# Performance work log

Measured on AMD Instinct MI355X. Metric: run time of the kernel, lower is better.

The kernel has to match this reference:

```python
import jax, jax.numpy as jnp
import numpy as np

DIM = 1024
D_SRC = 1024
H = 16
HD = DIM // H
SCALE = 1.0 / np.sqrt(DIM)  # module uses 1/sqrt(internal_dim), not head_dim


def setup_inputs() -> dict:
    key = jax.random.key(0)
    ks = jax.random.split(key, 7)
    B, T = 2, 2048
    Q = jax.random.normal(ks[0], (B, T, DIM), dtype=jnp.float32)
    K = jax.random.normal(ks[1], (B, T, D_SRC), dtype=jnp.float32)
    V = jax.random.normal(ks[2], (B, T, D_SRC), dtype=jnp.float32)
    # torch nn.Linear weights: (out_features, in_features); y = x @ W.T
    s = 0.02
    Wq = jax.random.normal(ks[3], (DIM, DIM), dtype=jnp.float32) * s
    Wk = jax.random.normal(ks[4], (DIM, D_SRC), dtype=jnp.float32) * s
    Wv = jax.random.normal(ks[5], (DIM, D_SRC), dtype=jnp.float32) * s
    Wo = jax.random.normal(ks[6], (DIM, DIM), dtype=jnp.float32) * s
    return {"Q": Q, "K": K, "V": V, "Wq": Wq, "Wk": Wk, "Wv": Wv, "Wo": Wo}


def _split_heads(x):  # (B,T,DIM) -> (B,H,T,HD)
    B, T, _ = x.shape
    return x.reshape(B, T, H, HD).transpose(0, 2, 1, 3)


def reference(Q, K, V, Wq, Wk, Wv, Wo):
    B, T, _ = Q.shape
    q = _split_heads(Q @ Wq.T)
    k = _split_heads(K @ Wk.T)
    v = _split_heads(V @ Wv.T)
    att = jnp.einsum('bhid,bhjd->bhij', q, k) * SCALE
    causal = jnp.tril(jnp.ones((T, T), dtype=bool))
    att = jnp.where(causal[None, None], att, -jnp.inf)
    att = jax.nn.softmax(att, axis=-1)
    y = jnp.einsum('bhij,bhjd->bhid', att, v)
    y = y.transpose(0, 2, 1, 3).reshape(B, T, DIM)
    y = y @ Wo.T
    return y, att
```

## Files before the change

kernel.cpp:

```cpp
#include <hip/hip_runtime.h>
#include <hip/hip_bf16.h>

#define Bb 2
#define Tt 2048
#define DIMd 1024
#define Hh 16
#define HDh 64
#define MTOK (Bb * Tt)
#define NSCALE 0.03125f

typedef __attribute__((ext_vector_type(8))) short bf16x8;
typedef __attribute__((ext_vector_type(4))) float floatx4;

__device__ __forceinline__ unsigned short f2bf(float f) {
    union { float f; unsigned int u; } a; a.f = f;
    const unsigned int u = a.u;
    return (unsigned short)((u + 0x7FFFu + ((u >> 16) & 1u)) >> 16);
}

__device__ __forceinline__ void gl_lds16(const void* g, void* l) {
    __builtin_amdgcn_global_load_lds((const __attribute__((address_space(1))) void*)g,
                                     (__attribute__((address_space(3))) void*)l, 16, 0, 0);
}

__global__ __launch_bounds__(256) void cvt_all(
    const float* __restrict__ s0, const float* __restrict__ s1, const float* __restrict__ s2,
    const float* __restrict__ s3, const float* __restrict__ s4, const float* __restrict__ s5,
    const float* __restrict__ s6,
    unsigned short* __restrict__ d0, unsigned short* __restrict__ d1, unsigned short* __restrict__ d2,
    unsigned short* __restrict__ d3, unsigned short* __restrict__ d4, unsigned short* __restrict__ d5,
    unsigned short* __restrict__ d6) {
    const int blk = blockIdx.x;
    const float* src; unsigned short* dst; int rb;
    if (blk < 12288) {
        const int r = blk >> 12;
        rb  = blk & 4095;
        src = (r == 0) ? s0 : ((r == 1) ? s1 : s2);
        dst = (r == 0) ? d0 : ((r == 1) ? d1 : d2);
    } else {
        const int r = (blk - 12288) >> 10;
        rb  = blk & 1023;
        src = (r == 0) ? s3 : ((r == 1) ? s4 : ((r == 2) ? s5 : s6));
        dst = (r == 0) ? d3 : ((r == 1) ? d4 : ((r == 2) ? d5 : d6));
    }
    const int i = (rb * 256 + threadIdx.x) * 4;
    const float4 v = *(const float4*)(src + i);
    ushort4 o;
    o.x = f2bf(v.x); o.y = f2bf(v.y); o.z = f2bf(v.z); o.w = f2bf(v.w);
    *(ushort4*)(dst + i) = o;
}

template <int BF16OUT>
__device__ __forceinline__ void gemm_tile(unsigned short* As, unsigned short* Bs,
                                          const unsigned short* __restrict__ A,
                                          const unsigned short* __restrict__ W,
                                          void* __restrict__ Cv,
                                          int N, int K, int m0, int n0) {
    const int tid  = threadIdx.x;
    const int wave = tid >> 6;
    const int lane = tid & 63;
    const int wm = (wave >> 1) * 64;
    const int wn = (wave & 1) * 64;
    const int qd = lane >> 4;
    const int ln16 = lane & 15;
    const int x7 = ln16 & 7;

    floatx4 acc[4][4];
#pragma unroll
    for (int mi = 0; mi < 4; ++mi)
#pragma unroll
        for (int ni = 0; ni < 4; ++ni) acc[mi][ni] = (floatx4){0.f, 0.f, 0.f, 0.f};

    for (int k0 = 0; k0 < K; k0 += 64) {
#pragma unroll
        for (int t = 0; t < 4; ++t) {
            const int c   = t * 256 + wave * 64 + lane;
            const int row = c >> 3;
            const int col = ((c & 7) ^ (row & 7)) * 8;
            gl_lds16(A + (size_t)(m0 + row) * K + k0 + col, &As[c * 8]);
            gl_lds16(W + (size_t)(n0 + row) * K + k0 + col, &Bs[c * 8]);
        }
        __syncthreads();

#pragma unroll
        for (int ks = 0; ks < 2; ++ks) {
            bf16x8 af[4], bfr[4];
#pragma unroll
            for (int mi = 0; mi < 4; ++mi)
                af[mi] = *(const bf16x8*)&As[(wm + mi * 16 + ln16) * 64 + (((ks * 4 + qd) ^ x7) * 8)];
#pragma unroll
            for (int ni = 0; ni < 4; ++ni)
                bfr[ni] = *(const bf16x8*)&Bs[(wn + ni * 16 + ln16) * 64 + (((ks * 4 + qd) ^ x7) * 8)];
            __builtin_amdgcn_s_setprio(1);
#pragma unroll
            for (int mi = 0; mi < 4; ++mi)
#pragma unroll
                for (int ni = 0; ni < 4; ++ni)
                    acc[mi][ni] = __builtin_amdgcn_mfma_f32_16x16x32_bf16(af[mi], bfr[ni], acc[mi][ni], 0, 0, 0);
            __builtin_amdgcn_s_setprio(0);
        }
        __syncthreads();
    }

#pragma unroll
    for (int mi = 0; mi < 4; ++mi)
#pragma unroll
        for (int ni = 0; ni < 4; ++ni) {
            const int gn = n0 + wn + ni * 16 + ln16;
#pragma unroll
            for (int r = 0; r < 4; ++r) {
                const int gm = m0 + wm + mi * 16 + qd * 4 + r;
                if (BF16OUT)
                    ((unsigned short*)Cv)[(size_t)gm * N + gn] = f2bf(acc[mi][ni][r]);
                else
                    ((float*)Cv)[(size_t)gm * N + gn] = acc[mi][ni][r];
            }
        }
}

__global__ __launch_bounds__(256) void gemm_proj3(
    const unsigned short* __restrict__ Qb, const unsigned short* __restrict__ Wqb, unsigned short* __restrict__ qp,
    const unsigned short* __restrict__ Kb, const unsigned short* __restrict__ Wkb, unsigned short* __restrict__ kp,
    const unsigned short* __restrict__ Vb, const unsigned short* __restrict__ Wvb, unsigned short* __restrict__ vt) {
    __shared__ unsigned short As[128 * 64];
    __shared__ unsigned short Bs[128 * 64];
    const int bid = blockIdx.x;
    if (bid < 256) {
        gemm_tile<1>(As, Bs, Qb, Wqb, qp, DIMd, DIMd, (bid >> 3) * 128, (bid & 7) * 128);
    } else if (bid < 512) {
        const int r = bid - 256;
        gemm_tile<1>(As, Bs, Kb, Wkb, kp, DIMd, DIMd, (r >> 3) * 128, (r & 7) * 128);
    } else {
        const int r = bid - 512;
        gemm_tile<1>(As, Bs, Wvb, Vb, vt, MTOK, DIMd, (r >> 5) * 128, (r & 31) * 128);
    }
}

__global__ __launch_bounds__(256) void gemm_o_rescale(const unsigned short* __restrict__ ymid,
                                                      const unsigned short* __restrict__ Wob,
                                                      float* __restrict__ y,
                                                      float* __restrict__ att,
                                                      const float* __restrict__ lws) {
    __shared__ unsigned short As[128 * 64];
    __shared__ unsigned short Bs[128 * 64];
    const int bid = blockIdx.x;
    if (bid < 256) {
        gemm_tile<0>(As, Bs, ymid, Wob, y, DIMd, DIMd, (bid >> 3) * 128, (bid & 7) * 128);
        return;
    }
    const int rb  = bid - 256;
    const int tid = threadIdx.x;
#pragma unroll
    for (int rr = 0; rr < 16; ++rr) {
        const int row = rb * 16 + rr;
        const int i   = row & (Tt - 1);
        const float inv = 1.f / lws[row];
        float4* arow = (float4*)(att + (size_t)row * Tt);
#pragma unroll
        for (int q = 0; q < 2; ++q) {
            const int f4 = tid + q * 256;
            const int j  = f4 * 4;
            float4 v;
            if (j <= i) {
                v = arow[f4];
                v.x = (j + 0 <= i) ? v.x * inv : 0.f;
                v.y = (j + 1 <= i) ? v.y * inv : 0.f;
                v.z = (j + 2 <= i) ? v.z * inv : 0.f;
                v.w = (j + 3 <= i) ? v.w * inv : 0.f;
            } else {
                v = make_float4(0.f, 0.f, 0.f, 0.f);
            }
            arow[f4] = v;
        }
    }
}

#define PSTR 72

__global__ __launch_bounds__(256) void fused_attn(const unsigned short* __restrict__ qp,
                                                  const unsigned short* __restrict__ kp,
                                                  const unsigned short* __restrict__ vt,
                                                  float* __restrict__ att,
                                                  unsigned short* __restrict__ ymid,
                                                  float* __restrict__ lws) {
    __shared__ unsigned short Ks[64 * 64];
    __shared__ unsigned short Vs[64 * 64];
    __shared__ unsigned short Ps[64 * PSTR];

    const int bid = blockIdx.x;
    const int bh  = bid & 31;
    const int it  = 31 - (bid >> 5);
    const int h   = bh & (Hh - 1);
    const int b   = bh >> 4;
    const int tid  = threadIdx.x;
    const int w    = tid >> 6;
    const int lane = tid & 63;
    const int qd   = lane >> 4;
    const int ln16 = lane & 15;
    const int i0   = it * 64;
    const int ig   = i0 + w * 16 + ln16;

    bf16x8 qf[2];
    {
        const unsigned short* qrow = qp + (size_t)(b * Tt + ig) * DIMd + h * HDh;
        qf[0] = *(const bf16x8*)(qrow + qd * 8);
        qf[1] = *(const bf16x8*)(qrow + 32 + qd * 8);
    }

    floatx4 oacc[4];
#pragma unroll
    for (int dt = 0; dt < 4; ++dt) oacc[dt] = (floatx4){0.f, 0.f, 0.f, 0.f};
    float lsum = 0.f;

    unsigned short* Pw = &Ps[w * 16 * PSTR];
    float* arow = att + ((size_t)bh * Tt + ig) * Tt;

    for (int jt = 0; jt <= it; ++jt) {
        const int j0 = jt * 64;
        __syncthreads();

#pragma unroll
        for (int t = 0; t < 2; ++t) {
            const int c   = w * 128 + t * 64 + lane;
            const int row = c >> 3;
            const int cb  = c & 7;
            const int col8 = ((cb ^ (row & 7)) * 8);
            gl_lds16(kp + (size_t)(b * Tt + j0 + row) * DIMd + h * HDh + col8, &Ks[c * 8]);
            gl_lds16(vt + (size_t)(h * HDh + row) * MTOK + b * Tt + j0 + col8, &Vs[c * 8]);
        }
        __syncthreads();

        floatx4 sacc[4];
#pragma unroll
        for (int ct = 0; ct < 4; ++ct) sacc[ct] = (floatx4){0.f, 0.f, 0.f, 0.f};
        __builtin_amdgcn_s_setprio(1);
#pragma unroll
        for (int ks = 0; ks < 2; ++ks)
#pragma unroll
            for (int ct = 0; ct < 4; ++ct) {
                const int row = ct * 16 + ln16;
                const bf16x8 kf = *(const bf16x8*)&Ks[row * 64 + (((ks * 4 + qd) ^ (row & 7)) * 8)];
                sacc[ct] = __builtin_amdgcn_mfma_f32_16x16x32_bf16(kf, qf[ks], sacc[ct], 0, 0, 0);
            }
        __builtin_amdgcn_s_setprio(0);

        float rs = 0.f;
#pragma unroll
        for (int ct = 0; ct < 4; ++ct) {
            const int jb = j0 + ct * 16 + qd * 4;
            float4 ev;
            {
                const float e0 = (jb + 0 <= ig) ? __expf(sacc[ct][0] * NSCALE) : 0.f;
                const float e1 = (jb + 1 <= ig) ? __expf(sacc[ct][1] * NSCALE) : 0.f;
                const float e2 = (jb + 2 <= ig) ? __expf(sacc[ct][2] * NSCALE) : 0.f;
                const float e3 = (jb + 3 <= ig) ? __expf(sacc[ct][3] * NSCALE) : 0.f;
                ev = make_float4(e0, e1, e2, e3);
                rs += e0 + e1 + e2 + e3;
            }
            *(float4*)(arow + jb) = ev;
            ushort4 pk;
            pk.x = f2bf(ev.x); pk.y = f2bf(ev.y); pk.z = f2bf(ev.z); pk.w = f2bf(ev.w);
            *(ushort4*)&Pw[ln16 * PSTR + ct * 16 + qd * 4] = pk;
        }
        rs += __shfl_xor(rs, 16);
        rs += __shfl_xor(rs, 32);
        lsum += rs;

        __builtin_amdgcn_s_setprio(1);
#pragma unroll
        for (int ks = 0; ks < 2; ++ks) {
            const bf16x8 pf = *(const bf16x8*)&Pw[ln16 * PSTR + ks * 32 + qd * 8];
#pragma unroll
            for (int dt = 0; dt < 4; ++dt) {
                const int row = dt * 16 + ln16;
                const bf16x8 vf = *(const bf16x8*)&Vs[row * 64 + (((ks * 4 + qd) ^ (row & 7)) * 8)];
                oacc[dt] = __builtin_amdgcn_mfma_f32_16x16x32_bf16(pf, vf, oacc[dt], 0, 0, 0);
            }
        }
        __builtin_amdgcn_s_setprio(0);
    }

    float lssrc[4];
#pragma unroll
    for (int r = 0; r < 4; ++r) lssrc[r] = __shfl(lsum, qd * 4 + r);
#pragma unroll
    for (int r = 0; r < 4; ++r) {
        const float inv = 1.f / lssrc[r];
        unsigned short* yr = ymid + (size_t)(b * Tt + i0 + w * 16 + qd * 4 + r) * DIMd + h * HDh + ln16;
#pragma unroll
        for (int dt = 0; dt < 4; ++dt)
            yr[dt * 16] = f2bf(oacc[dt][r] * inv);
    }
    if (qd == 0) lws[(size_t)bh * Tt + ig] = lsum;
}

extern "C" void kernel_launch(void* const* d_in, const int* in_sizes, int n_in,
                              void* d_out, int out_size, void* d_ws, size_t ws_size,
                              hipStream_t stream) {
    const float* Q  = (const float*)d_in[0];
    const float* K  = (const float*)d_in[1];
    const float* V  = (const float*)d_in[2];
    const float* Wq = (const float*)d_in[3];
    const float* Wk = (const float*)d_in[4];
    const float* Wv = (const float*)d_in[5];
    const float* Wo = (const float*)d_in[6];

    const size_t nytok = (size_t)Bb * Tt * DIMd;
    const size_t nw    = (size_t)DIMd * DIMd;
    float* y   = (float*)d_out;
    float* att = y + nytok;

    char* w = (char*)d_ws;
    unsigned short* qp  = (unsigned short*)w;    w += nytok * 2;
    unsigned short* kp  = (unsigned short*)w;    w += nytok * 2;
    unsigned short* vt  = (unsigned short*)w;    w += nytok * 2;
    unsigned short* Qb  = (unsigned short*)w;    w += nytok * 2;
    unsigned short* Kb  = (unsigned short*)w;    w += nytok * 2;
    unsigned short* Vb  = (unsigned short*)w;    w += nytok * 2;
    unsigned short* Wqb = (unsigned short*)w;    w += nw * 2;
    unsigned short* Wkb = (unsigned short*)w;    w += nw * 2;
    unsigned short* Wvb = (unsigned short*)w;    w += nw * 2;
    unsigned short* Wob = (unsigned short*)w;    w += nw * 2;
    float* lws = (float*)w;
    unsigned short* ymid_b = Qb;

    cvt_all<<<16384, 256, 0, stream>>>(Q, K, V, Wq, Wk, Wv, Wo,
                                       Qb, Kb, Vb, Wqb, Wkb, Wvb, Wob);

    gemm_proj3<<<768, 256, 0, stream>>>(Qb, Wqb, qp, Kb, Wkb, kp, Vb, Wvb, vt);

    fused_attn<<<32 * 32, 256, 0, stream>>>(qp, kp, vt, att, ymid_b, lws);

    gemm_o_rescale<<<256 + 4096, 256, 0, stream>>>(ymid_b, Wob, y, att, lws);
}
```

Before: 848.7 us.

## Recompute attention weights in final kernel instead of writing then rescaling

The attention kernel no longer writes unnormalised probabilities to the large att buffer. A new pass beside the output GEMM recomputes QK^T per 128x128 tile, applies exp and the stored row-sum inverse, and writes normalised weights once, zero-filling the upper triangle. This replaces a write, read and rewrite of the 512MB att tensor with a single write, at the cost of extra MFMA work. The GEMM tile also changes to a K-step of 32 with no LDS swizzle and no setprio, which may bring bank conflicts.

```diff
diff --git a/kernel.cpp b/kernel.cpp
--- a/kernel.cpp
+++ b/kernel.cpp
@@ -51,11 +51,11 @@
 }
 
 template <int BF16OUT>
-__device__ __forceinline__ void gemm_tile(unsigned short* As, unsigned short* Bs,
-                                          const unsigned short* __restrict__ A,
-                                          const unsigned short* __restrict__ W,
-                                          void* __restrict__ Cv,
-                                          int N, int K, int m0, int n0) {
+__device__ __forceinline__ void gemm_tile32(unsigned short* As, unsigned short* Bs,
+                                            const unsigned short* __restrict__ A,
+                                            const unsigned short* __restrict__ W,
+                                            void* __restrict__ Cv,
+                                            int N, int K, int m0, int n0) {
     const int tid  = threadIdx.x;
     const int wave = tid >> 6;
     const int lane = tid & 63;
@@ -63,7 +63,6 @@
     const int wn = (wave & 1) * 64;
     const int qd = lane >> 4;
     const int ln16 = lane & 15;
-    const int x7 = ln16 & 7;
 
     floatx4 acc[4][4];
 #pragma unroll
@@ -71,34 +70,29 @@
 #pragma unroll
         for (int ni = 0; ni < 4; ++ni) acc[mi][ni] = (floatx4){0.f, 0.f, 0.f, 0.f};
 
-    for (int k0 = 0; k0 < K; k0 += 64) {
-#pragma unroll
-        for (int t = 0; t < 4; ++t) {
-            const int c   = t * 256 + wave * 64 + lane;
-            const int row = c >> 3;
-            const int col = ((c & 7) ^ (row & 7)) * 8;
+    for (int k0 = 0; k0 < K; k0 += 32) {
+#pragma unroll
+        for (int t = 0; t < 2; ++t) {
+            const int c = t * 256 + wave * 64 + lane;
+            const int row = c >> 2;
+            const int col = (c & 3) * 8;
             gl_lds16(A + (size_t)(m0 + row) * K + k0 + col, &As[c * 8]);
             gl_lds16(W + (size_t)(n0 + row) * K + k0 + col, &Bs[c * 8]);
         }
         __syncthreads();
 
-#pragma unroll
-        for (int ks = 0; ks < 2; ++ks) {
-            bf16x8 af[4], bfr[4];
-#pragma unroll
-            for (int mi = 0; mi < 4; ++mi)
-                af[mi] = *(const bf16x8*)&As[(wm + mi * 16 + ln16) * 64 + (((ks * 4 + qd) ^ x7) * 8)];
+        bf16x8 af[4], bfr[4];
+#pragma unroll
+        for (int mi = 0; mi < 4; ++mi)
+            af[mi] = *(const bf16x8*)&As[(wm + mi * 16 + ln16) * 32 + qd * 8];
+#pragma unroll
+        for (int ni = 0; ni < 4; ++ni)
+            bfr[ni] = *(const bf16x8*)&Bs[(wn + ni * 16 + ln16) * 32 + qd * 8];
+#pragma unroll
+        for (int mi = 0; mi < 4; ++mi)
 #pragma unroll
             for (int ni = 0; ni < 4; ++ni)
-                bfr[ni] = *(const bf16x8*)&Bs[(wn + ni * 16 + ln16) * 64 + (((ks * 4 + qd) ^ x7) * 8)];
-            __builtin_amdgcn_s_setprio(1);
-#pragma unroll
-            for (int mi = 0; mi < 4; ++mi)
-#pragma unroll
-                for (int ni = 0; ni < 4; ++ni)
-                    acc[mi][ni] = __builtin_amdgcn_mfma_f32_16x16x32_bf16(af[mi], bfr[ni], acc[mi][ni], 0, 0, 0);
-            __builtin_amdgcn_s_setprio(0);
-        }
+                acc[mi][ni] = __builtin_amdgcn_mfma_f32_16x16x32_bf16(af[mi], bfr[ni], acc[mi][ni], 0, 0, 0);
         __syncthreads();
     }
 
@@ -122,56 +116,17 @@
     const unsigned short* __restrict__ Qb, const unsigned short* __restrict__ Wqb, unsigned short* __restrict__ qp,
     const unsigned short* __restrict__ Kb, const unsigned short* __restrict__ Wkb, unsigned short* __restrict__ kp,
     const unsigned short* __restrict__ Vb, const unsigned short* __restrict__ Wvb, unsigned short* __restrict__ vt) {
-    __shared__ unsigned short As[128 * 64];
-    __shared__ unsigned short Bs[128 * 64];
+    __shared__ unsigned short As[128 * 32];
+    __shared__ unsigned short Bs[128 * 32];
     const int bid = blockIdx.x;
     if (bid < 256) {
-        gemm_tile<1>(As, Bs, Qb, Wqb, qp, DIMd, DIMd, (bid >> 3) * 128, (bid & 7) * 128);
+        gemm_tile32<1>(As, Bs, Qb, Wqb, qp, DIMd, DIMd, (bid >> 3) * 128, (bid & 7) * 128);
     } else if (bid < 512) {
         const int r = bid - 256;
-        gemm_tile<1>(As, Bs, Kb, Wkb, kp, DIMd, DIMd, (r >> 3) * 128, (r & 7) * 128);
+        gemm_tile32<1>(As, Bs, Kb, Wkb, kp, DIMd, DIMd, (r >> 3) * 128, (r & 7) * 128);
     } else {
         const int r = bid - 512;
-        gemm_tile<1>(As, Bs, Wvb, Vb, vt, MTOK, DIMd, (r >> 5) * 128, (r & 31) * 128);
-    }
-}
-
-__global__ __launch_bounds__(256) void gemm_o_rescale(const unsigned short* __restrict__ ymid,
-                                                      const unsigned short* __restrict__ Wob,
-                                                      float* __restrict__ y,
-                                                      float* __restrict__ att,
-                                                      const float* __restrict__ lws) {
-    __shared__ unsigned short As[128 * 64];
-    __shared__ unsigned short Bs[128 * 64];
-    const int bid = blockIdx.x;
-    if (bid < 256) {
-        gemm_tile<0>(As, Bs, ymid, Wob, y, DIMd, DIMd, (bid >> 3) * 128, (bid & 7) * 128);
-        return;
-    }
-    const int rb  = bid - 256;
-    const int tid = threadIdx.x;
-#pragma unroll
-    for (int rr = 0; rr < 16; ++rr) {
-        const int row = rb * 16 + rr;
-        const int i   = row & (Tt - 1);
-        const float inv = 1.f / lws[row];
-        float4* arow = (float4*)(att + (size_t)row * Tt);
-#pragma unroll
-        for (int q = 0; q < 2; ++q) {
-            const int f4 = tid + q * 256;
-            const int j  = f4 * 4;
-            float4 v;
-            if (j <= i) {
-                v = arow[f4];
-                v.x = (j + 0 <= i) ? v.x * inv : 0.f;
-                v.y = (j + 1 <= i) ? v.y * inv : 0.f;
-                v.z = (j + 2 <= i) ? v.z * inv : 0.f;
-                v.w = (j + 3 <= i) ? v.w * inv : 0.f;
-            } else {
-                v = make_float4(0.f, 0.f, 0.f, 0.f);
-            }
-            arow[f4] = v;
-        }
+        gemm_tile32<1>(As, Bs, Wvb, Vb, vt, MTOK, DIMd, (r >> 5) * 128, (r & 31) * 128);
     }
 }
 
@@ -180,7 +135,6 @@
 __global__ __launch_bounds__(256) void fused_attn(const unsigned short* __restrict__ qp,
                                                   const unsigned short* __restrict__ kp,
                                                   const unsigned short* __restrict__ vt,
-                                                  float* __restrict__ att,
                                                   unsigned short* __restrict__ ymid,
                                                   float* __restrict__ lws) {
     __shared__ unsigned short Ks[64 * 64];
@@ -213,7 +167,6 @@
     float lsum = 0.f;
 
     unsigned short* Pw = &Ps[w * 16 * PSTR];
-    float* arow = att + ((size_t)bh * Tt + ig) * Tt;
 
     for (int jt = 0; jt <= it; ++jt) {
         const int j0 = jt * 64;
@@ -248,18 +201,13 @@
 #pragma unroll
         for (int ct = 0; ct < 4; ++ct) {
             const int jb = j0 + ct * 16 + qd * 4;
-            float4 ev;
-            {
-                const float e0 = (jb + 0 <= ig) ? __expf(sacc[ct][0] * NSCALE) : 0.f;
-                const float e1 = (jb + 1 <= ig) ? __expf(sacc[ct][1] * NSCALE) : 0.f;
-                const float e2 = (jb + 2 <= ig) ? __expf(sacc[ct][2] * NSCALE) : 0.f;
-                const float e3 = (jb + 3 <= ig) ? __expf(sacc[ct][3] * NSCALE) : 0.f;
-                ev = make_float4(e0, e1, e2, e3);
-                rs += e0 + e1 + e2 + e3;
-            }
-            *(float4*)(arow + jb) = ev;
+            const float e0 = (jb + 0 <= ig) ? __expf(sacc[ct][0] * NSCALE) : 0.f;
+            const float e1 = (jb + 1 <= ig) ? __expf(sacc[ct][1] * NSCALE) : 0.f;
+            const float e2 = (jb + 2 <= ig) ? __expf(sacc[ct][2] * NSCALE) : 0.f;
+            const float e3 = (jb + 3 <= ig) ? __expf(sacc[ct][3] * NSCALE) : 0.f;
+            rs += e0 + e1 + e2 + e3;
             ushort4 pk;
-            pk.x = f2bf(ev.x); pk.y = f2bf(ev.y); pk.z = f2bf(ev.z); pk.w = f2bf(ev.w);
+            pk.x = f2bf(e0); pk.y = f2bf(e1); pk.z = f2bf(e2); pk.w = f2bf(e3);
             *(ushort4*)&Pw[ln16 * PSTR + ct * 16 + qd * 4] = pk;
         }
         rs += __shfl_xor(rs, 16);
@@ -292,6 +240,104 @@
             yr[dt * 16] = f2bf(oacc[dt][r] * inv);
     }
     if (qd == 0) lws[(size_t)bh * Tt + ig] = lsum;
+}
+
+__global__ __launch_bounds__(256) void gemm_o_attw(const unsigned short* __restrict__ ymid,
+                                                   const unsigned short* __restrict__ Wob,
+                                                   float* __restrict__ y,
+                                                   const unsigned short* __restrict__ qp,
+                                                   const unsigned short* __restrict__ kp,
+                                                   const float* __restrict__ lws,
+                                                   float* __restrict__ att) {
+    __shared__ unsigned short smem[128 * 64];
+
+    const int bid = blockIdx.x;
+    if (bid < 256) {
+        gemm_tile32<0>(smem, smem + 128 * 32, ymid, Wob, y, DIMd, DIMd,
+                       (bid >> 3) * 128, (bid & 7) * 128);
+        return;
+    }
+    const int ab = bid - 256;
+    const int bh = ab >> 8;
+    const int t  = ab & 255;
+    const int ti = t >> 4;
+    const int tj = t & 15;
+    const int h  = bh & (Hh - 1);
+    const int b  = bh >> 4;
+    const int tid = threadIdx.x;
+    const int i0 = ti * 128;
+    const int j0 = tj * 128;
+    float* abase = att + (size_t)bh * Tt * Tt;
+
+    if (tj > ti) {
+        const float4 z = make_float4(0.f, 0.f, 0.f, 0.f);
+#pragma unroll
+        for (int k = 0; k < 16; ++k) {
+            const int f   = k * 256 + tid;
+            const int row = f >> 5;
+            const int c4  = f & 31;
+            *(float4*)(abase + (size_t)(i0 + row) * Tt + j0 + c4 * 4) = z;
+        }
+        return;
+    }
+
+    const int w    = tid >> 6;
+    const int lane = tid & 63;
+    const int qd   = lane >> 4;
+    const int ln16 = lane & 15;
+    const int wm   = (w >> 1) * 64;
+    const int wn   = (w & 1) * 64;
+
+#pragma unroll
+    for (int t4 = 0; t4 < 4; ++t4) {
+        const int c   = t4 * 256 + tid;
+        const int row = c >> 3;
+        const int cb  = c & 7;
+        const int col8 = ((cb ^ (row & 7)) * 8);
+        gl_lds16(kp + (size_t)(b * Tt + j0 + row) * DIMd + h * HDh + col8, &smem[c * 8]);
+    }
+
+    bf16x8 qf[4][2];
+    float linv[4];
+#pragma unroll
+    for (int qt = 0; qt < 4; ++qt) {
+        const int iq = i0 + wm + qt * 16 + ln16;
+        const unsigned short* qrow = qp + (size_t)(b * Tt + iq) * DIMd + h * HDh;
+        qf[qt][0] = *(const bf16x8*)(qrow + qd * 8);
+        qf[qt][1] = *(const bf16x8*)(qrow + 32 + qd * 8);
+        linv[qt]  = 1.f / lws[(size_t)bh * Tt + iq];
+    }
+    __syncthreads();
+
+    const bool diag = (ti == tj);
+#pragma unroll
+    for (int ct = 0; ct < 4; ++ct) {
+        const int krow = wn + ct * 16 + ln16;
+        const bf16x8 kf0 = *(const bf16x8*)&smem[krow * 64 + ((qd ^ (krow & 7)) * 8)];
+        const bf16x8 kf1 = *(const bf16x8*)&smem[krow * 64 + (((4 + qd) ^ (krow & 7)) * 8)];
+#pragma unroll
+        for (int qt = 0; qt < 4; ++qt) {
+            floatx4 s = (floatx4){0.f, 0.f, 0.f, 0.f};
+            s = __builtin_amdgcn_mfma_f32_16x16x32_bf16(kf0, qf[qt][0], s, 0, 0, 0);
+            s = __builtin_amdgcn_mfma_f32_16x16x32_bf16(kf1, qf[qt][1], s, 0, 0, 0);
+            const int ig = i0 + wm + qt * 16 + ln16;
+            const int jb = j0 + wn + ct * 16 + qd * 4;
+            const float il = linv[qt];
+            float4 ev;
+            if (diag) {
+                ev.x = (jb + 0 <= ig) ? __expf(s[0] * NSCALE) * il : 0.f;
+                ev.y = (jb + 1 <= ig) ? __expf(s[1] * NSCALE) * il : 0.f;
+                ev.z = (jb + 2 <= ig) ? __expf(s[2] * NSCALE) * il : 0.f;
+                ev.w = (jb + 3 <= ig) ? __expf(s[3] * NSCALE) * il : 0.f;
+            } else {
+                ev.x = __expf(s[0] * NSCALE) * il;
+                ev.y = __expf(s[1] * NSCALE) * il;
+                ev.z = __expf(s[2] * NSCALE) * il;
+                ev.w = __expf(s[3] * NSCALE) * il;
+            }
+            *(float4*)(abase + (size_t)ig * Tt + jb) = ev;
+        }
+    }
 }
 
 extern "C" void kernel_launch(void* const* d_in, const int* in_sizes, int n_in,
@@ -329,7 +375,7 @@
 
     gemm_proj3<<<768, 256, 0, stream>>>(Qb, Wqb, qp, Kb, Wkb, kp, Vb, Wvb, vt);
 
-    fused_attn<<<32 * 32, 256, 0, stream>>>(qp, kp, vt, att, ymid_b, lws);
-
-    gemm_o_rescale<<<256 + 4096, 256, 0, stream>>>(ymid_b, Wob, y, att, lws);
-}
+    fused_attn<<<32 * 32, 256, 0, stream>>>(qp, kp, vt, ymid_b, lws);
+
+    gemm_o_attw<<<256 + 8192, 256, 0, stream>>>(ymid_b, Wob, y, qp, kp, lws, att);
+}
```

Measured after the change: 711.5 us. 1.19x faster.
